# Kernel tuning notes

Hardware: AMD Instinct MI355X
Metric: run time of the kernel (lower is better)

The kernel has to match this reference:

```python
import jax, jax.numpy as jnp
import numpy as np
import math

B, CIN, H, W = 32, 128, 64, 64
COUT, KH, KW = 256, 3, 3


def setup_inputs() -> dict:
    key = jax.random.key(0)
    k1, k2, k3 = jax.random.split(key, 3)
    sqrtk = math.sqrt(1.0 / (CIN * KH * KW))
    x = jax.random.normal(k1, (B, CIN, H, W), dtype=jnp.float32)
    weight = jax.random.uniform(k2, (COUT, CIN, KH, KW), dtype=jnp.float32, minval=-sqrtk, maxval=sqrtk)
    bias = jax.random.uniform(k3, (COUT,), dtype=jnp.float32, minval=-sqrtk, maxval=sqrtk)
    return {"input": x, "weight": weight, "bias": bias}


def reference(input, weight, bias):
    # VALID (no padding), stride-1 cross-correlation conv, NCHW/OIHW layout,
    # matching the original nested-loop direct convolution + per-channel bias.
    out = jax.lax.conv_general_dilated(
        input, weight,
        window_strides=(1, 1), padding='VALID',
        dimension_numbers=('NCHW', 'OIHW', 'NCHW'))
    return out + bias[None, :, None, None]
```

## Files before the change

kernel.cpp:

```cpp
#include <hip/hip_runtime.h>

#define NB   32
#define NCI  128
#define NH   64
#define NW   64
#define NCO  256
#define NOH  62
#define NOW  62

typedef __attribute__((ext_vector_type(8))) short bf16x8;
typedef __attribute__((ext_vector_type(8))) unsigned short u16x8;
typedef __attribute__((ext_vector_type(4))) float f32x4;

typedef __attribute__((address_space(1))) const unsigned int glb_u32_t;
typedef __attribute__((address_space(3))) unsigned int lds_u32_t;

__device__ __forceinline__ unsigned short f2bf(float f) {
  unsigned int u = __float_as_uint(f);
  u = u + 0x7FFFu + ((u >> 16) & 1u);
  return (unsigned short)(u >> 16);
}

__device__ __forceinline__ void gload_lds16(const unsigned short* g, unsigned short* l) {
  __builtin_amdgcn_global_load_lds((glb_u32_t*)g, (lds_u32_t*)l, 16, 0, 0);
}

__global__ __launch_bounds__(256) void cvt_x_kernel(const float* __restrict__ x,
                                                    unsigned short* __restrict__ xt) {
  __shared__ unsigned short l[64 * 130];
  const int tid = threadIdx.x;
  const int b = blockIdx.x >> 6, h = blockIdx.x & 63;
  const int w0 = tid & 63, c0 = tid >> 6;
  const float* src = x + ((size_t)b * NCI * NH + h) * NW;
  #pragma unroll
  for (int g = 0; g < 32; ++g) {
    int ci = g * 4 + c0;
    l[w0 * 130 + ci] = f2bf(src[(size_t)ci * (NH * NW) + w0]);
  }
  __syncthreads();
  unsigned short* dst = xt + ((size_t)b * NH + h) * NW * NCI;
  #pragma unroll
  for (int it = 0; it < 4; ++it) {
    int gidx = it * 2048 + tid * 8;
    int w = gidx >> 7, ci0 = gidx & 127;
    const unsigned int* lw = (const unsigned int*)(l + w * 130 + ci0);
    union { u16x8 v; unsigned int u[4]; } t;
    t.u[0] = lw[0]; t.u[1] = lw[1]; t.u[2] = lw[2]; t.u[3] = lw[3];
    *(u16x8*)(dst + w * NCI + ci0) = t.v;
  }
}

__global__ __launch_bounds__(256) void cvt_w_kernel(const float* __restrict__ wsrc,
                                                    unsigned short* __restrict__ wt) {
  int t = blockIdx.x * 256 + threadIdx.x;
  int oc = t & 15, co = (t >> 4) & 255, k = t >> 12;
  const float* src = wsrc + ((size_t)co * NCI + oc * 8) * 9 + k;
  u16x8 v;
  #pragma unroll
  for (int j = 0; j < 8; ++j) v[j] = f2bf(src[j * 9]);
  *(u16x8*)(wt + ((size_t)k * NCO + co) * NCI + oc * 8) = v;
}

__global__ __launch_bounds__(256, 2) void conv_mfma_kernel(
    const unsigned short* __restrict__ xt, const unsigned short* __restrict__ wt,
    const float* __restrict__ bias, float* __restrict__ out) {
  __shared__ unsigned short smem[40960];

  const int tid  = threadIdx.x;
  const int lane = tid & 63;
  const int wid  = tid >> 6;
  const int wn   = wid;
  const int l15  = lane & 15;
  const int lo   = lane >> 4;

  const int bid0  = blockIdx.x;
  const int bid   = (bid0 & 7) * 128 + (bid0 >> 3);
  const int coutg = bid & 1;
  const int ohg   = (bid >> 1) & 15;
  const int b     = bid >> 5;
  const int cbase = coutg * 128;
  const int oh0   = ohg * 4;

  f32x4 acc[8][4];
  #pragma unroll
  for (int mi = 0; mi < 8; ++mi)
    #pragma unroll
    for (int ni = 0; ni < 4; ++ni)
      acc[mi][ni] = (f32x4){0.f, 0.f, 0.f, 0.f};

  const char* sm = (const char*)smem;
  const int af_lane = l15 * 64 + ((lo ^ ((l15 >> 1) & 3)) << 4);

  const size_t xbase = (size_t)b * NH * NW * NCI;
  const unsigned short* xsrc[6];
  #pragma unroll
  for (int i = 0; i < 6; ++i) {
    int e = (wid * 6 + i) * 64 + lane;
    int o = e & 3, w = (e >> 2) & 63, r = e >> 8;
    int row = oh0 + r; if (row > 63) row = 63;
    xsrc[i] = xt + xbase + ((size_t)row * NW + w) * NCI
            + ((o ^ ((w >> 1) & 3)) * 8);
  }
  const unsigned short* wsrc2[2];
  #pragma unroll
  for (int i = 0; i < 2; ++i) {
    int e = (wid * 2 + i) * 64 + lane;
    int o = e & 3, co = e >> 2;
    wsrc2[i] = wt + (size_t)(cbase + co) * NCI + ((o ^ ((co >> 1) & 3)) * 8);
  }

  auto stage_w = [&](int t) {
    unsigned short* dst = smem + 24576 + (t & 3) * 4096;
    const size_t so = (size_t)(t % 9) * NCO * NCI + (t / 9) * 32;
    #pragma unroll
    for (int i = 0; i < 2; ++i)
      gload_lds16(wsrc2[i] + so, dst + ((wid * 2 + i) * 64 + lane) * 8);
  };
  auto stage_x = [&](int c) {
    unsigned short* dst = smem + (c & 1) * 12288;
    #pragma unroll
    for (int i = 0; i < 6; ++i)
      gload_lds16(xsrc[i] + c * 32, dst + ((wid * 6 + i) * 64 + lane) * 8);
  };

  bf16x8 afX[4], afY[4], bfC[4], bfD[4];

  auto tap_body = [&](int t, bf16x8 (&bfc)[4], bf16x8 (&bfn)[4], bool pf) {
    const int t9 = t % 9, c = t / 9;
    const bool xst = (t9 == 5) && (c < 3);
    if (t + 3 < 36) stage_w(t + 3);
    if (xst) stage_x(c + 1);

    const char* wsp = sm + 49152 + (t & 3) * 8192;
    const int  tn   = t + 1;
    const char* wspn = sm + 49152 + (tn & 3) * 8192;
    const int  tn9 = tn % 9, cn = tn / 9;
    const int  khn = tn9 / 3, kwn = tn9 - khn * 3;
    const char* xspn = sm + (cn & 1) * 24576 + (wn + khn) * 4096;
    const int  w9n  = l15 + kwn;
    const int  bfln = w9n * 64 + ((lo ^ ((w9n >> 1) & 3)) << 4);

    asm volatile("s_waitcnt lgkmcnt(0)" ::: "memory");
    __builtin_amdgcn_sched_barrier(0);
    __builtin_amdgcn_s_setprio(1);
    #pragma unroll
    for (int ni = 0; ni < 4; ++ni)
      acc[0][ni] = __builtin_amdgcn_mfma_f32_16x16x32_bf16(afX[0], bfc[ni], acc[0][ni], 0, 0, 0);
    afY[0] = *(const bf16x8*)(wsp + 4 * 1024 + af_lane);
    afY[1] = *(const bf16x8*)(wsp + 5 * 1024 + af_lane);
    #pragma unroll
    for (int ni = 0; ni < 4; ++ni)
      acc[1][ni] = __builtin_amdgcn_mfma_f32_16x16x32_bf16(afX[1], bfc[ni], acc[1][ni], 0, 0, 0);
    afY[2] = *(const bf16x8*)(wsp + 6 * 1024 + af_lane);
    afY[3] = *(const bf16x8*)(wsp + 7 * 1024 + af_lane);
    #pragma unroll
    for (int ni = 0; ni < 4; ++ni)
      acc[2][ni] = __builtin_amdgcn_mfma_f32_16x16x32_bf16(afX[2], bfc[ni], acc[2][ni], 0, 0, 0);
    #pragma unroll
    for (int ni = 0; ni < 4; ++ni)
      acc[3][ni] = __builtin_amdgcn_mfma_f32_16x16x32_bf16(afX[3], bfc[ni], acc[3][ni], 0, 0, 0);
    __builtin_amdgcn_s_setprio(0);

    asm volatile("s_waitcnt lgkmcnt(0)" ::: "memory");
    __builtin_amdgcn_sched_barrier(0);
    __builtin_amdgcn_s_setprio(1);
    #pragma unroll
    for (int ni = 0; ni < 4; ++ni)
      acc[4][ni] = __builtin_amdgcn_mfma_f32_16x16x32_bf16(afY[0], bfc[ni], acc[4][ni], 0, 0, 0);
    if (pf) {
      afX[0] = *(const bf16x8*)(wspn + 0 * 1024 + af_lane);
      afX[1] = *(const bf16x8*)(wspn + 1 * 1024 + af_lane);
    }
    #pragma unroll
    for (int ni = 0; ni < 4; ++ni)
      acc[5][ni] = __builtin_amdgcn_mfma_f32_16x16x32_bf16(afY[1], bfc[ni], acc[5][ni], 0, 0, 0);
    if (pf) {
      afX[2] = *(const bf16x8*)(wspn + 2 * 1024 + af_lane);
      afX[3] = *(const bf16x8*)(wspn + 3 * 1024 + af_lane);
    }
    #pragma unroll
    for (int ni = 0; ni < 4; ++ni)
      acc[6][ni] = __builtin_amdgcn_mfma_f32_16x16x32_bf16(afY[2], bfc[ni], acc[6][ni], 0, 0, 0);
    if (pf) {
      #pragma unroll
      for (int i = 0; i < 4; ++i)
        bfn[i] = *(const bf16x8*)(xspn + i * 1024 + bfln);
    }
    #pragma unroll
    for (int ni = 0; ni < 4; ++ni)
      acc[7][ni] = __builtin_amdgcn_mfma_f32_16x16x32_bf16(afY[3], bfc[ni], acc[7][ni], 0, 0, 0);
    __builtin_amdgcn_s_setprio(0);

    if (t >= 33) {
      asm volatile("s_waitcnt vmcnt(0)" ::: "memory");
    } else if ((t9 == 5 || t9 == 6) && c < 3) {
      asm volatile("s_waitcnt vmcnt(8)" ::: "memory");
    } else {
      asm volatile("s_waitcnt vmcnt(2)" ::: "memory");
    }
    __builtin_amdgcn_s_barrier();
    __builtin_amdgcn_sched_barrier(0);
  };

  stage_w(0);
  stage_w(1);
  stage_w(2);
  stage_x(0);
  asm volatile("s_waitcnt vmcnt(0)" ::: "memory");
  __builtin_amdgcn_s_barrier();
  __builtin_amdgcn_sched_barrier(0);
  {
    const char* wsp0 = sm + 49152;
    #pragma unroll
    for (int i = 0; i < 4; ++i)
      afX[i] = *(const bf16x8*)(wsp0 + i * 1024 + af_lane);
    const char* xsp0 = sm + wn * 4096;
    #pragma unroll
    for (int i = 0; i < 4; ++i)
      bfC[i] = *(const bf16x8*)(xsp0 + i * 1024 + af_lane);
  }

  for (int j = 0; j < 9; ++j) {
    const int t0 = 4 * j;
    tap_body(t0 + 0, bfC, bfD, true);
    tap_body(t0 + 1, bfD, bfC, true);
    tap_body(t0 + 2, bfC, bfD, true);
    tap_body(t0 + 3, bfD, bfC, j < 8);
  }

  const int oh = oh0 + wn;
  if (oh < NOH) {
    #pragma unroll
    for (int mi = 0; mi < 8; ++mi) {
      int co0 = cbase + mi * 16 + lo * 4;
      const f32x4 bv = *(const f32x4*)(bias + co0);
      #pragma unroll
      for (int ni = 0; ni < 4; ++ni) {
        int ow = ni * 16 + l15;
        if (ow < NOW) {
          size_t o0 = (((size_t)b * NCO + co0) * NOH + oh) * NOW + ow;
          const size_t cs = (size_t)NOH * NOW;
          out[o0]          = acc[mi][ni][0] + bv[0];
          out[o0 + cs]     = acc[mi][ni][1] + bv[1];
          out[o0 + 2 * cs] = acc[mi][ni][2] + bv[2];
          out[o0 + 3 * cs] = acc[mi][ni][3] + bv[3];
        }
      }
    }
  }
}

__global__ __launch_bounds__(256) void conv_naive_kernel(
    const float* __restrict__ x, const float* __restrict__ w,
    const float* __restrict__ bias, float* __restrict__ out) {
  long t = (long)blockIdx.x * 256 + threadIdx.x;
  const long total = (long)NB * NCO * NOH * NOW;
  if (t >= total) return;
  int ow = (int)(t % NOW);
  int oh = (int)((t / NOW) % NOH);
  int co = (int)((t / ((long)NOW * NOH)) % NCO);
  int b  = (int)(t / ((long)NOW * NOH * NCO));
  float acc = bias[co];
  for (int ci = 0; ci < NCI; ++ci) {
    const float* xp = x + (((size_t)b * NCI + ci) * NH + oh) * NW + ow;
    const float* wp = w + ((size_t)co * NCI + ci) * 9;
    #pragma unroll
    for (int kh = 0; kh < 3; ++kh)
      #pragma unroll
      for (int kw = 0; kw < 3; ++kw)
        acc += xp[kh * NW + kw] * wp[kh * 3 + kw];
  }
  out[t] = acc;
}

extern "C" void kernel_launch(void* const* d_in, const int* in_sizes, int n_in,
                              void* d_out, int out_size, void* d_ws, size_t ws_size,
                              hipStream_t stream) {
  const float* x    = (const float*)d_in[0];
  const float* w    = (const float*)d_in[1];
  const float* bias = (const float*)d_in[2];
  float* out        = (float*)d_out;

  const size_t WT_BYTES = (size_t)9 * NCO * NCI * 2;
  const size_t XT_BYTES = (size_t)NB * NH * NW * NCI * 2;

  if (ws_size >= WT_BYTES + XT_BYTES) {
    unsigned short* wt = (unsigned short*)d_ws;
    unsigned short* xt = (unsigned short*)((char*)d_ws + WT_BYTES);
    cvt_w_kernel<<<(9 * NCO * 16) / 256, 256, 0, stream>>>(w, wt);
    cvt_x_kernel<<<NB * NH, 256, 0, stream>>>(x, xt);
    conv_mfma_kernel<<<2 * 16 * NB, 256, 0, stream>>>(xt, wt, bias, out);
  } else {
    const long total = (long)NB * NCO * NOH * NOW;
    conv_naive_kernel<<<(int)((total + 255) / 256), 256, 0, stream>>>(x, w, bias, out);
  }
}
```

Before: 95.08 us.

## Fuse fp32-to-bf16 input transpose into conv kernel's LDS staging

```diff
diff --git a/kernel.cpp b/kernel.cpp
--- a/kernel.cpp
+++ b/kernel.cpp
@@ -23,31 +23,6 @@
 
 __device__ __forceinline__ void gload_lds16(const unsigned short* g, unsigned short* l) {
   __builtin_amdgcn_global_load_lds((glb_u32_t*)g, (lds_u32_t*)l, 16, 0, 0);
-}
-
-__global__ __launch_bounds__(256) void cvt_x_kernel(const float* __restrict__ x,
-                                                    unsigned short* __restrict__ xt) {
-  __shared__ unsigned short l[64 * 130];
-  const int tid = threadIdx.x;
-  const int b = blockIdx.x >> 6, h = blockIdx.x & 63;
-  const int w0 = tid & 63, c0 = tid >> 6;
-  const float* src = x + ((size_t)b * NCI * NH + h) * NW;
-  #pragma unroll
-  for (int g = 0; g < 32; ++g) {
-    int ci = g * 4 + c0;
-    l[w0 * 130 + ci] = f2bf(src[(size_t)ci * (NH * NW) + w0]);
-  }
-  __syncthreads();
-  unsigned short* dst = xt + ((size_t)b * NH + h) * NW * NCI;
-  #pragma unroll
-  for (int it = 0; it < 4; ++it) {
-    int gidx = it * 2048 + tid * 8;
-    int w = gidx >> 7, ci0 = gidx & 127;
-    const unsigned int* lw = (const unsigned int*)(l + w * 130 + ci0);
-    union { u16x8 v; unsigned int u[4]; } t;
-    t.u[0] = lw[0]; t.u[1] = lw[1]; t.u[2] = lw[2]; t.u[3] = lw[3];
-    *(u16x8*)(dst + w * NCI + ci0) = t.v;
-  }
 }
 
 __global__ __launch_bounds__(256) void cvt_w_kernel(const float* __restrict__ wsrc,
@@ -62,7 +37,7 @@
 }
 
 __global__ __launch_bounds__(256, 2) void conv_mfma_kernel(
-    const unsigned short* __restrict__ xt, const unsigned short* __restrict__ wt,
+    const float* __restrict__ x, const unsigned short* __restrict__ wt,
     const float* __restrict__ bias, float* __restrict__ out) {
   __shared__ unsigned short smem[40960];
 
@@ -91,16 +66,8 @@
   const char* sm = (const char*)smem;
   const int af_lane = l15 * 64 + ((lo ^ ((l15 >> 1) & 3)) << 4);
 
-  const size_t xbase = (size_t)b * NH * NW * NCI;
-  const unsigned short* xsrc[6];
-  #pragma unroll
-  for (int i = 0; i < 6; ++i) {
-    int e = (wid * 6 + i) * 64 + lane;
-    int o = e & 3, w = (e >> 2) & 63, r = e >> 8;
-    int row = oh0 + r; if (row > 63) row = 63;
-    xsrc[i] = xt + xbase + ((size_t)row * NW + w) * NCI
-            + ((o ^ ((w >> 1) & 3)) * 8);
-  }
+  const float* xb = x + ((size_t)b * NCI) * (NH * NW);
+
   const unsigned short* wsrc2[2];
   #pragma unroll
   for (int i = 0; i < 2; ++i) {
@@ -116,49 +83,82 @@
     for (int i = 0; i < 2; ++i)
       gload_lds16(wsrc2[i] + so, dst + ((wid * 2 + i) * 64 + lane) * 8);
   };
-  auto stage_x = [&](int c) {
-    unsigned short* dst = smem + (c & 1) * 12288;
-    #pragma unroll
-    for (int i = 0; i < 6; ++i)
-      gload_lds16(xsrc[i] + c * 32, dst + ((wid * 6 + i) * 64 + lane) * 8);
+
+  auto xload8 = [&](int c1, int uu, float (&xf)[8]) {
+    const int g = uu * 4 + wid;
+    const int r = g % 6, oct = g / 6;
+    int row = oh0 + r; if (row > 63) row = 63;
+    const float* src = xb + (size_t)(c1 * 32 + oct * 8) * (NH * NW)
+                     + row * NW + lane;
+    #pragma unroll
+    for (int j = 0; j < 8; ++j) xf[j] = src[(size_t)j * (NH * NW)];
   };
-
-  bf16x8 afX[4], afY[4], bfC[4], bfD[4];
-
-  auto tap_body = [&](int t, bf16x8 (&bfc)[4], bf16x8 (&bfn)[4], bool pf) {
+  auto xwrite8 = [&](int c1, int uu, float (&xf)[8]) {
+    const int g = uu * 4 + wid;
+    const int r = g % 6, oct = g / 6;
+    u16x8 v;
+    #pragma unroll
+    for (int j = 0; j < 8; ++j) v[j] = f2bf(xf[j]);
+    *(u16x8*)(smem + (c1 & 1) * 12288 +
+              ((r * 64 + lane) * 4 + (oct ^ ((lane >> 1) & 3))) * 8) = v;
+  };
+
+  bf16x8 afX[4], afY[4], bfC[4];
+
+  {
+    float xa[8], xbv[8], xc[8], xd[8], xe[8], xg[8];
+    xload8(0, 0, xa); xload8(0, 1, xbv); xload8(0, 2, xc);
+    xload8(0, 3, xd); xload8(0, 4, xe);  xload8(0, 5, xg);
+    stage_w(0); stage_w(1); stage_w(2);
+    asm volatile("s_waitcnt vmcnt(6)" ::: "memory");
+    xwrite8(0, 0, xa); xwrite8(0, 1, xbv); xwrite8(0, 2, xc);
+    xwrite8(0, 3, xd); xwrite8(0, 4, xe);  xwrite8(0, 5, xg);
+    asm volatile("s_waitcnt vmcnt(0) lgkmcnt(0)" ::: "memory");
+    __builtin_amdgcn_s_barrier();
+    __builtin_amdgcn_sched_barrier(0);
+    const char* wsp0 = sm + 49152;
+    #pragma unroll
+    for (int i = 0; i < 4; ++i)
+      afX[i] = *(const bf16x8*)(wsp0 + i * 1024 + af_lane);
+    const char* xsp0 = sm + wn * 4096;
+    #pragma unroll
+    for (int i = 0; i < 4; ++i)
+      bfC[i] = *(const bf16x8*)(xsp0 + i * 1024 + af_lane);
+  }
+
+  for (int t = 0; t < 36; ++t) {
     const int t9 = t % 9, c = t / 9;
-    const bool xst = (t9 == 5) && (c < 3);
+    const bool xst = (t9 >= 2 && t9 <= 7) && (c < 3);
+    const bool pf  = (t < 35);
+    float xf[8];
+
+    if (xst) xload8(c + 1, t9 - 2, xf);
+    __builtin_amdgcn_sched_barrier(0);
     if (t + 3 < 36) stage_w(t + 3);
-    if (xst) stage_x(c + 1);
-
-    const char* wsp = sm + 49152 + (t & 3) * 8192;
-    const int  tn   = t + 1;
-    const char* wspn = sm + 49152 + (tn & 3) * 8192;
-    const int  tn9 = tn % 9, cn = tn / 9;
-    const int  khn = tn9 / 3, kwn = tn9 - khn * 3;
-    const char* xspn = sm + (cn & 1) * 24576 + (wn + khn) * 4096;
-    const int  w9n  = l15 + kwn;
-    const int  bfln = w9n * 64 + ((lo ^ ((w9n >> 1) & 3)) << 4);
+    __builtin_amdgcn_sched_barrier(0);
+
+    const char* wsp  = sm + 49152 + (t & 3) * 8192;
+    const char* wspn = sm + 49152 + ((t + 1) & 3) * 8192;
 
     asm volatile("s_waitcnt lgkmcnt(0)" ::: "memory");
     __builtin_amdgcn_sched_barrier(0);
     __builtin_amdgcn_s_setprio(1);
     #pragma unroll
     for (int ni = 0; ni < 4; ++ni)
-      acc[0][ni] = __builtin_amdgcn_mfma_f32_16x16x32_bf16(afX[0], bfc[ni], acc[0][ni], 0, 0, 0);
+      acc[0][ni] = __builtin_amdgcn_mfma_f32_16x16x32_bf16(afX[0], bfC[ni], acc[0][ni], 0, 0, 0);
     afY[0] = *(const bf16x8*)(wsp + 4 * 1024 + af_lane);
     afY[1] = *(const bf16x8*)(wsp + 5 * 1024 + af_lane);
     #pragma unroll
     for (int ni = 0; ni < 4; ++ni)
-      acc[1][ni] = __builtin_amdgcn_mfma_f32_16x16x32_bf16(afX[1], bfc[ni], acc[1][ni], 0, 0, 0);
+      acc[1][ni] = __builtin_amdgcn_mfma_f32_16x16x32_bf16(afX[1], bfC[ni], acc[1][ni], 0, 0, 0);
     afY[2] = *(const bf16x8*)(wsp + 6 * 1024 + af_lane);
     afY[3] = *(const bf16x8*)(wsp + 7 * 1024 + af_lane);
     #pragma unroll
     for (int ni = 0; ni < 4; ++ni)
-      acc[2][ni] = __builtin_amdgcn_mfma_f32_16x16x32_bf16(afX[2], bfc[ni], acc[2][ni], 0, 0, 0);
-    #pragma unroll
-    for (int ni = 0; ni < 4; ++ni)
-      acc[3][ni] = __builtin_amdgcn_mfma_f32_16x16x32_bf16(afX[3], bfc[ni], acc[3][ni], 0, 0, 0);
+      acc[2][ni] = __builtin_amdgcn_mfma_f32_16x16x32_bf16(afX[2], bfC[ni], acc[2][ni], 0, 0, 0);
+    #pragma unroll
+    for (int ni = 0; ni < 4; ++ni)
+      acc[3][ni] = __builtin_amdgcn_mfma_f32_16x16x32_bf16(afX[3], bfC[ni], acc[3][ni], 0, 0, 0);
     __builtin_amdgcn_s_setprio(0);
 
     asm volatile("s_waitcnt lgkmcnt(0)" ::: "memory");
@@ -166,66 +166,45 @@
     __builtin_amdgcn_s_setprio(1);
     #pragma unroll
     for (int ni = 0; ni < 4; ++ni)
-      acc[4][ni] = __builtin_amdgcn_mfma_f32_16x16x32_bf16(afY[0], bfc[ni], acc[4][ni], 0, 0, 0);
+      acc[4][ni] = __builtin_amdgcn_mfma_f32_16x16x32_bf16(afY[0], bfC[ni], acc[4][ni], 0, 0, 0);
     if (pf) {
       afX[0] = *(const bf16x8*)(wspn + 0 * 1024 + af_lane);
       afX[1] = *(const bf16x8*)(wspn + 1 * 1024 + af_lane);
     }
     #pragma unroll
     for (int ni = 0; ni < 4; ++ni)
-      acc[5][ni] = __builtin_amdgcn_mfma_f32_16x16x32_bf16(afY[1], bfc[ni], acc[5][ni], 0, 0, 0);
+      acc[5][ni] = __builtin_amdgcn_mfma_f32_16x16x32_bf16(afY[1], bfC[ni], acc[5][ni], 0, 0, 0);
     if (pf) {
       afX[2] = *(const bf16x8*)(wspn + 2 * 1024 + af_lane);
       afX[3] = *(const bf16x8*)(wspn + 3 * 1024 + af_lane);
     }
     #pragma unroll
     for (int ni = 0; ni < 4; ++ni)
-      acc[6][ni] = __builtin_amdgcn_mfma_f32_16x16x32_bf16(afY[2], bfc[ni], acc[6][ni], 0, 0, 0);
+      acc[6][ni] = __builtin_amdgcn_mfma_f32_16x16x32_bf16(afY[2], bfC[ni], acc[6][ni], 0, 0, 0);
+    #pragma unroll
+    for (int ni = 0; ni < 4; ++ni)
+      acc[7][ni] = __builtin_amdgcn_mfma_f32_16x16x32_bf16(afY[3], bfC[ni], acc[7][ni], 0, 0, 0);
+    __builtin_amdgcn_s_setprio(0);
+
+    if (t >= 33) {
+      asm volatile("s_waitcnt vmcnt(0)" ::: "memory");
+    } else {
+      asm volatile("s_waitcnt vmcnt(2)" ::: "memory");
+    }
+    if (xst) xwrite8(c + 1, t9 - 2, xf);
     if (pf) {
+      const int tn = t + 1, tn9 = tn % 9, cn = tn / 9;
+      const int khn = tn9 / 3, kwn = tn9 - khn * 3;
+      const char* xspn = sm + (cn & 1) * 24576 + (wn + khn) * 4096;
+      const int w9n = l15 + kwn;
+      const int bfln = w9n * 64 + ((lo ^ ((w9n >> 1) & 3)) << 4);
       #pragma unroll
       for (int i = 0; i < 4; ++i)
-        bfn[i] = *(const bf16x8*)(xspn + i * 1024 + bfln);
-    }
-    #pragma unroll
-    for (int ni = 0; ni < 4; ++ni)
-      acc[7][ni] = __builtin_amdgcn_mfma_f32_16x16x32_bf16(afY[3], bfc[ni], acc[7][ni], 0, 0, 0);
-    __builtin_amdgcn_s_setprio(0);
-
-    if (t >= 33) {
-      asm volatile("s_waitcnt vmcnt(0)" ::: "memory");
-    } else if ((t9 == 5 || t9 == 6) && c < 3) {
-      asm volatile("s_waitcnt vmcnt(8)" ::: "memory");
-    } else {
-      asm volatile("s_waitcnt vmcnt(2)" ::: "memory");
-    }
+        bfC[i] = *(const bf16x8*)(xspn + i * 1024 + bfln);
+    }
+    if (xst) asm volatile("s_waitcnt lgkmcnt(4)" ::: "memory");
     __builtin_amdgcn_s_barrier();
     __builtin_amdgcn_sched_barrier(0);
-  };
-
-  stage_w(0);
-  stage_w(1);
-  stage_w(2);
-  stage_x(0);
-  asm volatile("s_waitcnt vmcnt(0)" ::: "memory");
-  __builtin_amdgcn_s_barrier();
-  __builtin_amdgcn_sched_barrier(0);
-  {
-    const char* wsp0 = sm + 49152;
-    #pragma unroll
-    for (int i = 0; i < 4; ++i)
-      afX[i] = *(const bf16x8*)(wsp0 + i * 1024 + af_lane);
-    const char* xsp0 = sm + wn * 4096;
-    #pragma unroll
-    for (int i = 0; i < 4; ++i)
-      bfC[i] = *(const bf16x8*)(xsp0 + i * 1024 + af_lane);
-  }
-
-  for (int j = 0; j < 9; ++j) {
-    const int t0 = 4 * j;
-    tap_body(t0 + 0, bfC, bfD, true);
-    tap_body(t0 + 1, bfD, bfC, true);
-    tap_body(t0 + 2, bfC, bfD, true);
-    tap_body(t0 + 3, bfD, bfC, j < 8);
   }
 
   const int oh = oh0 + wn;
@@ -282,14 +261,11 @@
   float* out        = (float*)d_out;
 
   const size_t WT_BYTES = (size_t)9 * NCO * NCI * 2;
-  const size_t XT_BYTES = (size_t)NB * NH * NW * NCI * 2;
-
-  if (ws_size >= WT_BYTES + XT_BYTES) {
+
+  if (ws_size >= WT_BYTES) {
     unsigned short* wt = (unsigned short*)d_ws;
-    unsigned short* xt = (unsigned short*)((char*)d_ws + WT_BYTES);
     cvt_w_kernel<<<(9 * NCO * 16) / 256, 256, 0, stream>>>(w, wt);
-    cvt_x_kernel<<<NB * NH, 256, 0, stream>>>(x, xt);
-    conv_mfma_kernel<<<2 * 16 * NB, 256, 0, stream>>>(xt, wt, bias, out);
+    conv_mfma_kernel<<<2 * 16 * NB, 256, 0, stream>>>(x, wt, bias, out);
   } else {
     const long total = (long)NB * NCO * NOH * NOW;
     conv_naive_kernel<<<(int)((total + 255) / 256), 256, 0, stream>>>(x, w, bias, out);
```

Measured after the change: 88.83 us. 6.6% less time.
